# Kernel tuning notes

Hardware: AMD Instinct MI355X
Metric: run time of the kernel (lower is better)

The kernel has to match this reference:

```python
import jax, jax.numpy as jnp
import numpy as np

NC = 10          # num_clusters
D_MODEL = 512
H = 8
DK = 64          # d_model = H*DK
B = 8
L = 2048


def _mlp2(x, W1, b1, W2, b2):
    h = jax.nn.gelu(x @ W1 + b1, approximate=False)
    return h @ W2 + b2


def setup_inputs() -> dict:
    key = jax.random.key(0)
    ks = jax.random.split(key, 12)
    s_in = 1.0 / np.sqrt(D_MODEL)
    s_h = 1.0 / np.sqrt(4 * NC)
    s_nc = 1.0 / np.sqrt(NC)
    return {
        "Q": jax.random.normal(ks[0], (B, H, L, DK), jnp.float32),
        "K": jax.random.normal(ks[1], (B, H, L, DK), jnp.float32),
        "V": jax.random.normal(ks[2], (B, H, L, DK), jnp.float32),
        # cluster_k_proj: Linear(d_model,4*nc) GELU Linear(4*nc,nc); stored as [in,out]
        "Wk1": jax.random.normal(ks[3], (D_MODEL, 4 * NC), jnp.float32) * s_in,
        "bk1": jnp.zeros((4 * NC,), jnp.float32),
        "Wk2": jax.random.normal(ks[4], (4 * NC, NC), jnp.float32) * s_h,
        "bk2": jnp.zeros((NC,), jnp.float32),
        # cluster_q_proj
        "Wq1": jax.random.normal(ks[5], (D_MODEL, 4 * NC), jnp.float32) * s_in,
        "bq1": jnp.zeros((4 * NC,), jnp.float32),
        "Wq2": jax.random.normal(ks[6], (4 * NC, NC), jnp.float32) * s_h,
        "bq2": jnp.zeros((NC,), jnp.float32),
        # proj_back_to_cluster_k: Linear(nc, d_model) + GELU
        "Wp": jax.random.normal(ks[7], (NC, D_MODEL), jnp.float32) * s_nc,
        "bp": jnp.zeros((D_MODEL,), jnp.float32),
    }


def _forward(Q, K, V, Wk1, bk1, Wk2, bk2, Wq1, bq1, Wq2, bq2, Wp, bp):
    b, h, l, d_k = Q.shape
    nc = Wk2.shape[1]
    unfolding = 10 * nc

    def pool(x):
        # torch: MaxPool1d(kernel=9, stride=9(default), padding=4) on reshape(b, d_k*h, -1)
        x3 = x.reshape(b, d_k * h, -1)
        y = jax.lax.reduce_window(x3, -jnp.inf, jax.lax.max,
                                  (1, 1, 9), (1, 1, 9),
                                  ((0, 0), (0, 0), (4, 4)))
        return y.reshape(b, h, -1, d_k)

    Kp = pool(K)
    Vp = pool(V)
    l_k = Kp.shape[2]

    # pad along batch dim and take sliding windows of size `unfolding` (stride 1)
    pad = jnp.zeros((unfolding, h, l_k, d_k), Kp.dtype)
    K_padded = jnp.concatenate([pad, Kp[1:]], axis=0)      # [unfolding+b-1, h, l_k, d_k]
    idx = jnp.arange(b)[:, None] + jnp.arange(unfolding)[None, :]
    K_unf = K_padded[idx]                                  # [b, unfolding, h, l_k, d_k]
    K_unf = jnp.transpose(K_unf, (0, 2, 3, 4, 1))          # torch unfold puts window last
    K_unf = K_unf.reshape(b, l_k, unfolding, d_k * h)      # row-major reshape, as torch

    ck = jax.nn.softmax(_mlp2(K_unf, Wk1, bk1, Wk2, bk2), axis=-1)  # [b,l_k,u,nc]
    cq = jax.nn.softmax(_mlp2(K_unf, Wq1, bq1, Wq2, bq2), axis=-1)

    mu = jnp.mean(cq, axis=-1)                             # [b, l_k, unfolding]
    sigma = jax.nn.softplus(jnp.std(cq, axis=-1, ddof=1))  # torch std is unbiased
    x = jnp.mean(ck, axis=-1)
    log_prob = -0.5 * jnp.square((x - mu) / sigma) - jnp.log(sigma) - 0.5 * jnp.log(2.0 * jnp.pi)
    # torch CrossEntropyLoss(mu, mu): classes are dim 1 (l_k), soft prob targets
    logp = jax.nn.log_softmax(mu, axis=1)
    ce = jnp.mean(-jnp.sum(mu * logp, axis=1))
    loss = -jnp.mean(log_prob) + ce

    # fused scatter-style cluster centers: mean over window of cq with assigned cluster zeroed
    assign = jnp.argmax(cq, axis=-1)                       # [b, l_k, unfolding]
    onehot = jax.nn.one_hot(assign, nc, dtype=cq.dtype)    # [b, l_k, u, i] (constant wrt grad)
    total = jnp.sum(cq, axis=2)                            # [b, l_k, nc]
    S = jnp.einsum('blui,bluc->blic', onehot, cq)          # sum of cq at masked positions
    centers = (total[:, :, None, :] - S) / unfolding       # [b, l_k, nc_i, nc_c]
    centers = jnp.transpose(centers, (2, 0, 1, 3))         # [nc, b, l_k, nc]

    cc = jax.nn.gelu(centers @ Wp + bp, approximate=False) # [nc, b, l_k, d_model]
    cc = cc.reshape(b, h, nc, l_k, d_k)                    # faithful torch reshape

    scores = jnp.einsum('bhqd,bhckd->bhqk', Q, cc) / np.sqrt(d_k).astype(Q.dtype)
    attn = jax.nn.softmax(scores, axis=-1)
    context = jnp.einsum('bhqk,bhkd->bhqd', attn, Vp)
    return context, loss


def reference(Q, K, V, Wk1, bk1, Wk2, bk2, Wq1, bq1, Wq2, bq2, Wp, bp):
    return _forward(Q, K, V, Wk1, bk1, Wk2, bk2, Wq1, bq1, Wq2, bq2, Wp, bp)
```

## Files before the change

kernel.cpp:

```cpp
#include <hip/hip_runtime.h>
#include <math.h>

#define NCL 10
#define DM 512
#define NH 8
#define DK 64
#define NB 8
#define SL 2048
#define LK 228
#define UF 100
#define KP_PER_B (NH*LK*DK)
#define KP_TOT (NB*KP_PER_B)
#define NROWS (NB*LK*UF)
#define POOL2_BLOCKS 8192

typedef __bf16 bf16_t;
typedef __attribute__((ext_vector_type(2))) __bf16 bf16x2;
typedef __attribute__((ext_vector_type(8))) __bf16 bf16x8;
typedef __attribute__((ext_vector_type(4))) float f32x4;

__device__ __forceinline__ float gelu_f(float x) {
    return 0.5f * x * (1.f + erff(x * 0.70710678118654752f));
}

__global__ void k_pool(const float* __restrict__ K, const float* __restrict__ V,
                       float* __restrict__ Kp, float* __restrict__ Vp,
                       const float* __restrict__ Wq1, bf16_t* __restrict__ W1b,
                       float* __restrict__ acc) {
    int bid = blockIdx.x;
    int tid = threadIdx.x;
    if (bid >= POOL2_BLOCKS) {
        int i = (bid - POOL2_BLOCKS) * 256 + tid;
        if (i < 512 * 40) W1b[i] = (bf16_t)Wq1[i];
        if (bid == POOL2_BLOCKS && tid < 4) acc[tid] = 0.f;
        return;
    }
    int kv = bid >> 12;
    int e0 = bid & 4095;
    int b = e0 >> 9;
    int c = e0 & 511;
    const float* src = kv ? V : K;
    float* dst = kv ? Vp : Kp;
    __shared__ float buf[2048];
    const float* base = src + (size_t)e0 * 2048;
    #pragma unroll
    for (int i = 0; i < 2; ++i) {
        int i4 = (tid + i * 256) << 2;
        *(float4*)&buf[i4] = *(const float4*)&base[i4];
    }
    __syncthreads();
    if (tid < LK) {
        int p0 = tid * 9 - 4;
        float mx = -3.4e38f;
        #pragma unroll
        for (int j = 0; j < 9; ++j) {
            int p = p0 + j;
            if (p >= 0 && p < 2048) mx = fmaxf(mx, buf[p]);
        }
        dst[b * KP_PER_B + c * LK + tid] = mx;
    }
}

template<int B>
__device__ __forceinline__ void layer1(int tid, const bf16_t* __restrict__ W1b,
                                       const float* __restrict__ Sstf,
                                       float* __restrict__ hT) {
    #pragma unroll 1
    for (int k = 0; k < 2; ++k) {
        int vt = tid + (k << 8);
        if (vt < 500) {
            int m = vt / 5;
            int h8 = vt - m * 5;
            int bm = (12 * m) % 100;
            float h[8];
            #pragma unroll
            for (int i = 0; i < 8; ++i) h[i] = 0.f;
            #pragma unroll
            for (int s = 1; s <= B; ++s) {
                const int t = 99 - B + s;
                int d0 = t - bm; if (d0 < 0) d0 += 100;
                int r0 = ((m << 9) + d0 - t) / 100;
                const float* srow = &Sstf[(s - 1) << 9];
                #pragma unroll
                for (int j = 0; j < 6; ++j) {
                    int c = d0 + j * 100;
                    if (j < 5 || c < 512) {
                        float v = srow[r0 + j];
                        bf16x8 w = *(const bf16x8*)&W1b[c * 40 + h8 * 8];
                        #pragma unroll
                        for (int i = 0; i < 8; ++i)
                            h[i] = fmaf(v, (float)w[i], h[i]);
                    }
                }
            }
            #pragma unroll
            for (int i = 0; i < 8; ++i) hT[m * 44 + h8 * 8 + i] = h[i];
        }
    }
}

__global__ __launch_bounds__(256, 4) void k_mlp(
        const float* __restrict__ Kp, const bf16_t* __restrict__ W1b,
        const float* __restrict__ bq1,
        const float* __restrict__ Wq2, const float* __restrict__ bq2,
        float* __restrict__ mu_g, float* __restrict__ centers_g,
        float* __restrict__ acc_g) {
    __shared__ __align__(16) char smem[32384];
    float* Sstf  = (float*)smem;
    float* hT    = (float*)(smem + 14336);
    float* stats = (float*)(smem + 31936);

    int tid = threadIdx.x;
    int bid = blockIdx.x;
    int b = bid & 7;
    int l = bid >> 3;
    int bl = b * LK + l;

    for (int s4 = tid; s4 < 128 * b; s4 += 256) {
        int bk = (s4 >> 7) + 1;
        int r4 = (s4 & 127) << 2;
        *(float4*)&Sstf[((bk - 1) << 9) + r4] =
            *(const float4*)&Kp[bk * KP_PER_B + l * 512 + r4];
    }
    if (tid < 111) stats[tid] = 0.f;
    if (b == 0) {
        for (int i = tid; i < 4400; i += 256) hT[i] = 0.f;
    }
    __syncthreads();

    switch (b) {
        case 1: layer1<1>(tid, W1b, Sstf, hT); break;
        case 2: layer1<2>(tid, W1b, Sstf, hT); break;
        case 3: layer1<3>(tid, W1b, Sstf, hT); break;
        case 4: layer1<4>(tid, W1b, Sstf, hT); break;
        case 5: layer1<5>(tid, W1b, Sstf, hT); break;
        case 6: layer1<6>(tid, W1b, Sstf, hT); break;
        case 7: layer1<7>(tid, W1b, Sstf, hT); break;
        default: break;
    }
    __syncthreads();

    for (int i = tid; i < 4000; i += 256) {
        int row = i / 40;
        int j = i - row * 40;
        hT[row * 44 + j] = gelu_f(hT[row * 44 + j] + bq1[j]);
    }
    __syncthreads();

    float* total_l = stats;
    float* S_l = stats + 10;
    float* lp_acc = stats + 110;

    if (tid < 100) {
        int row = tid;
        float g[40];
        #pragma unroll
        for (int j4 = 0; j4 < 10; ++j4) {
            float4 gv = *(const float4*)&hT[row * 44 + j4 * 4];
            g[j4 * 4 + 0] = gv.x; g[j4 * 4 + 1] = gv.y;
            g[j4 * 4 + 2] = gv.z; g[j4 * 4 + 3] = gv.w;
        }
        float out[10];
        #pragma unroll
        for (int c = 0; c < 10; ++c) out[c] = bq2[c];
        #pragma unroll
        for (int j = 0; j < 40; ++j) {
            float gj = g[j];
            #pragma unroll
            for (int c = 0; c < 10; ++c)
                out[c] = fmaf(gj, Wq2[j * 10 + c], out[c]);
        }
        float m = out[0]; int am = 0;
        #pragma unroll
        for (int c = 1; c < 10; ++c)
            if (out[c] > m) { m = out[c]; am = c; }
        float e[10], s = 0.f;
        #pragma unroll
        for (int c = 0; c < 10; ++c) { e[c] = expf(out[c] - m); s += e[c]; }
        float inv = 1.f / s;
        float cq[10], s1 = 0.f;
        #pragma unroll
        for (int c = 0; c < 10; ++c) { cq[c] = e[c] * inv; s1 += cq[c]; }
        float mean = s1 * 0.1f;
        float var = 0.f;
        #pragma unroll
        for (int c = 0; c < 10; ++c) { float d = cq[c] - mean; var += d * d; }
        float sd = sqrtf(var / 9.f);
        float sp = log1pf(expf(sd));
        float lp = -logf(sp) - 0.91893853320467274f;
        mu_g[bl * 100 + row] = mean;
        atomicAdd(lp_acc, lp);
        #pragma unroll
        for (int c = 0; c < 10; ++c) {
            atomicAdd(&total_l[c], cq[c]);
            atomicAdd(&S_l[am * 10 + c], cq[c]);
        }
    }
    __syncthreads();
    if (tid == 0) atomicAdd(&acc_g[0], lp_acc[0]);
    if (tid < 100) {
        centers_g[bl * 100 + tid] = (total_l[tid % 10] - S_l[tid]) * 0.01f;
    }
}

__global__ void k_ce(const float* __restrict__ mu_g, float* __restrict__ acc_g,
                     float* __restrict__ outp) {
    int bid = blockIdx.x;
    int b = bid / 100;
    int u = bid % 100;
    int lane = threadIdx.x;
    float v[4];
    #pragma unroll
    for (int t = 0; t < 4; ++t) {
        int l = lane + t * 64;
        v[t] = (l < LK) ? mu_g[(b * LK + l) * 100 + u] : -3.4e38f;
    }
    float m = fmaxf(fmaxf(v[0], v[1]), fmaxf(v[2], v[3]));
    for (int o = 32; o > 0; o >>= 1) m = fmaxf(m, __shfl_xor(m, o, 64));
    float se = 0.f;
    #pragma unroll
    for (int t = 0; t < 4; ++t) {
        int l = lane + t * 64;
        if (l < LK) se += expf(v[t] - m);
    }
    for (int o = 32; o > 0; o >>= 1) se += __shfl_xor(se, o, 64);
    float lse = m + logf(se);
    float dot = 0.f;
    #pragma unroll
    for (int t = 0; t < 4; ++t) {
        int l = lane + t * 64;
        if (l < LK) dot += v[t] * (v[t] - lse);
    }
    for (int o = 32; o > 0; o >>= 1) dot += __shfl_xor(dot, o, 64);
    if (lane == 0) {
        atomicAdd(&acc_g[1], -dot * (1.f / 800.f));
        __threadfence();
        unsigned int old = atomicAdd((unsigned int*)&acc_g[2], 1u);
        if (old == 799u) {
            __threadfence();
            outp[8388608] = -(acc_g[0] * (1.f / (float)NROWS)) + acc_g[1];
        }
    }
}

__global__ void k_ccs(const float* __restrict__ centers_g,
                      const float* __restrict__ Wp, const float* __restrict__ bp,
                      float* __restrict__ ccs) {
    int tid = blockIdx.x * 256 + threadIdx.x;
    if (tid >= KP_TOT) return;
    int k2d2 = tid % (LK * DK);
    int bh = tid / (LK * DK);
    float s = 0.f;
    #pragma unroll
    for (int i2 = 0; i2 < 10; ++i2) {
        int t2 = bh * 145920 + i2 * 14592 + k2d2;
        int i = t2 / 933888;
        int r1 = t2 % 933888;
        int bs = r1 / 116736;
        int r2 = r1 % 116736;
        int ls = r2 / 512;
        int mm = r2 % 512;
        const float* cen = centers_g + (bs * LK + ls) * 100 + i * 10;
        float val = bp[mm];
        #pragma unroll
        for (int c = 0; c < 10; ++c)
            val = fmaf(cen[c], Wp[c * 512 + mm], val);
        s += gelu_f(val);
    }
    ccs[tid] = s;
}

#define QT 128
__global__ __launch_bounds__(256, 3) void k_attn(
        const float* __restrict__ Q, const float* __restrict__ ccs,
        const float* __restrict__ Vp, float* __restrict__ outp) {
    __shared__ __align__(16) char smem[36864];
    bf16_t* Kl = (bf16_t*)(smem);
    bf16_t* Vt = (bf16_t*)(smem + 9216);
    bf16_t* Pl = (bf16_t*)(smem + 18432);

    int tid = threadIdx.x;
    int wid = tid >> 6;
    int lane = tid & 63;
    int ln = lane & 15;
    int qd = lane >> 4;
    int bid = blockIdx.x;
    int bh = bid >> 4;
    int qt = bid & 15;
    int qbase = qt * QT;

    const float* Qbh = Q + (size_t)bh * SL * DK;
    const float* Kbh = ccs + (size_t)bh * LK * DK;
    const float* Vbh = Vp + (size_t)bh * LK * DK;

    for (int s = tid; s < QT * 32; s += 256) {
        int r = s >> 5;
        int c2 = s & 31;
        float2 v = *(const float2*)&Qbh[(size_t)(qbase + r) * DK + c2 * 2];
        *(bf16x2*)&Pl[r * 72 + c2 * 2] = (bf16x2){(bf16_t)v.x, (bf16_t)v.y};
    }
    __syncthreads();
    bf16x8 qf[2][2];
    #pragma unroll
    for (int mt = 0; mt < 2; ++mt)
        #pragma unroll
        for (int ks = 0; ks < 2; ++ks)
            qf[mt][ks] = *(const bf16x8*)&Pl[(wid * 32 + mt * 16 + ln) * 72 + ks * 32 + qd * 8];

    f32x4 acc_o[2][4];
    float mrow[2][4], lrow[2][4];
    #pragma unroll
    for (int mt = 0; mt < 2; ++mt)
        #pragma unroll
        for (int t = 0; t < 4; ++t) {
            acc_o[mt][t] = (f32x4)(0.f);
            mrow[mt][t] = -3.0e38f;
            lrow[mt][t] = 0.f;
        }

    for (int ch = 0; ch < 4; ++ch) {
        int k0 = ch * 64;
        __syncthreads();
        for (int s = tid; s < 64 * 32; s += 256) {
            int kk = s >> 5;
            int c2 = s & 31;
            int key = k0 + kk;
            float2 v = (key < LK) ? *(const float2*)&Kbh[(size_t)key * DK + c2 * 2]
                                  : make_float2(0.f, 0.f);
            *(bf16x2*)&Kl[kk * 72 + c2 * 2] = (bf16x2){(bf16_t)v.x, (bf16_t)v.y};
        }
        for (int s = tid; s < 64 * 16; s += 256) {
            int kk = s >> 4;
            int c4 = s & 15;
            int key = k0 + kk;
            float4 v = (key < LK) ? *(const float4*)&Vbh[(size_t)key * DK + c4 * 4]
                                  : make_float4(0.f, 0.f, 0.f, 0.f);
            Vt[(c4 * 4 + 0) * 72 + kk] = (bf16_t)v.x;
            Vt[(c4 * 4 + 1) * 72 + kk] = (bf16_t)v.y;
            Vt[(c4 * 4 + 2) * 72 + kk] = (bf16_t)v.z;
            Vt[(c4 * 4 + 3) * 72 + kk] = (bf16_t)v.w;
        }
        __syncthreads();

        f32x4 accs[2][4];
        #pragma unroll
        for (int mt = 0; mt < 2; ++mt)
            #pragma unroll
            for (int nt = 0; nt < 4; ++nt) accs[mt][nt] = (f32x4)(0.f);
        #pragma unroll
        for (int ks = 0; ks < 2; ++ks) {
            #pragma unroll
            for (int nt = 0; nt < 4; ++nt) {
                bf16x8 bf = *(const bf16x8*)&Kl[(nt * 16 + ln) * 72 + ks * 32 + qd * 8];
                #pragma unroll
                for (int mt = 0; mt < 2; ++mt)
                    accs[mt][nt] = __builtin_amdgcn_mfma_f32_16x16x32_bf16(qf[mt][ks], bf, accs[mt][nt], 0, 0, 0);
            }
        }

        #pragma unroll
        for (int mt = 0; mt < 2; ++mt) {
            #pragma unroll
            for (int r = 0; r < 4; ++r) {
                float sv[4];
                #pragma unroll
                for (int nt = 0; nt < 4; ++nt) {
                    float s = accs[mt][nt][r] * 0.125f;
                    int key = k0 + nt * 16 + ln;
                    sv[nt] = (key < LK) ? s : -3.0e38f;
                }
                float rmax = fmaxf(fmaxf(sv[0], sv[1]), fmaxf(sv[2], sv[3]));
                #pragma unroll
                for (int o = 1; o < 16; o <<= 1)
                    rmax = fmaxf(rmax, __shfl_xor(rmax, o, 64));
                float mold = mrow[mt][r];
                float mnew = fmaxf(mold, rmax);
                float alpha = __expf(mold - mnew);
                float p[4], psum = 0.f;
                #pragma unroll
                for (int nt = 0; nt < 4; ++nt) {
                    p[nt] = __expf(sv[nt] - mnew);
                    psum += p[nt];
                }
                #pragma unroll
                for (int o = 1; o < 16; o <<= 1)
                    psum += __shfl_xor(psum, o, 64);
                lrow[mt][r] = lrow[mt][r] * alpha + psum;
                mrow[mt][r] = mnew;
                #pragma unroll
                for (int ntv = 0; ntv < 4; ++ntv)
                    acc_o[mt][ntv][r] *= alpha;
                int prow = (wid * 32 + mt * 16 + qd * 4 + r) * 72;
                #pragma unroll
                for (int nt = 0; nt < 4; ++nt)
                    Pl[prow + nt * 16 + ln] = (bf16_t)p[nt];
            }
        }

        #pragma unroll
        for (int ks = 0; ks < 2; ++ks) {
            bf16x8 pa[2];
            #pragma unroll
            for (int mt = 0; mt < 2; ++mt)
                pa[mt] = *(const bf16x8*)&Pl[(wid * 32 + mt * 16 + ln) * 72 + ks * 32 + qd * 8];
            #pragma unroll
            for (int ntv = 0; ntv < 4; ++ntv) {
                bf16x8 vb = *(const bf16x8*)&Vt[(ntv * 16 + ln) * 72 + ks * 32 + qd * 8];
                #pragma unroll
                for (int mt = 0; mt < 2; ++mt)
                    acc_o[mt][ntv] = __builtin_amdgcn_mfma_f32_16x16x32_bf16(pa[mt], vb, acc_o[mt][ntv], 0, 0, 0);
            }
        }
    }

    #pragma unroll
    for (int mt = 0; mt < 2; ++mt) {
        #pragma unroll
        for (int r = 0; r < 4; ++r) {
            float inv = 1.f / lrow[mt][r];
            int q_idx = qbase + wid * 32 + mt * 16 + qd * 4 + r;
            float* orow = outp + ((size_t)bh * SL + q_idx) * DK;
            #pragma unroll
            for (int ntv = 0; ntv < 4; ++ntv)
                orow[ntv * 16 + ln] = acc_o[mt][ntv][r] * inv;
        }
    }
}

extern "C" void kernel_launch(void* const* d_in, const int* in_sizes, int n_in,
                              void* d_out, int out_size, void* d_ws, size_t ws_size,
                              hipStream_t stream) {
    const float* Q   = (const float*)d_in[0];
    const float* K   = (const float*)d_in[1];
    const float* V   = (const float*)d_in[2];
    const float* Wq1 = (const float*)d_in[7];
    const float* bq1 = (const float*)d_in[8];
    const float* Wq2 = (const float*)d_in[9];
    const float* bq2 = (const float*)d_in[10];
    const float* Wp  = (const float*)d_in[11];
    const float* bp  = (const float*)d_in[12];
    float* out = (float*)d_out;

    float* ws      = (float*)d_ws;
    float* Kp      = ws;
    float* Vp      = ws + 933888;
    float* mu      = ws + 1867776;
    float* centers = ws + 2050176;
    float* ccs     = ws + 2232576;
    float* acc     = ws + 3166464;
    bf16_t* W1b    = (bf16_t*)(ws + 3166468);

    k_pool<<<POOL2_BLOCKS + 80, 256, 0, stream>>>(K, V, Kp, Vp, Wq1, W1b, acc);
    k_mlp<<<NB * LK, 256, 0, stream>>>(Kp, W1b, bq1, Wq2, bq2, mu, centers, acc);
    k_ccs<<<(KP_TOT + 255) / 256, 256, 0, stream>>>(centers, Wp, bp, ccs);
    k_ce<<<NB * 100, 64, 0, stream>>>(mu, acc, out);
    k_attn<<<NB * NH * (SL / QT), 256, 0, stream>>>(Q, ccs, Vp, out);
}
```

Before: 331.3 us.

## Fuse ccs and CE kernels, transpose mu layout, prescale Q, raise attn occupancy

Merges the ccs projection kernel and the cross-entropy kernel into one launch, with block ranges dispatching to each part. This removes one launch and lets the two independent pieces of work overlap. The mu buffer is stored transposed so the CE reduction reads it contiguously instead of with a stride of 100. The ccs index math now uses shifts and masks instead of divisions, and the 1/sqrt(dk) scale moves into the Q load so it leaves the inner loop. The attention kernel's launch bounds go from 3 to 4 blocks per SM, which may force register spills.

Measured after the change: 324.7 us. -2.0%, faster.

```diff
diff --git a/kernel.cpp b/kernel.cpp
--- a/kernel.cpp
+++ b/kernel.cpp
@@ -13,6 +13,8 @@
 #define KP_TOT (NB*KP_PER_B)
 #define NROWS (NB*LK*UF)
 #define POOL2_BLOCKS 8192
+#define KCCS_BLOCKS 3648
+#define KCE_BLOCKS 200
 
 typedef __bf16 bf16_t;
 typedef __attribute__((ext_vector_type(2))) __bf16 bf16x2;
@@ -188,7 +190,7 @@
         float sd = sqrtf(var / 9.f);
         float sp = log1pf(expf(sd));
         float lp = -logf(sp) - 0.91893853320467274f;
-        mu_g[bl * 100 + row] = mean;
+        mu_g[(b * 100 + row) * LK + l] = mean;
         atomicAdd(lp_acc, lp);
         #pragma unroll
         for (int c = 0; c < 10; ++c) {
@@ -203,17 +205,46 @@
     }
 }
 
-__global__ void k_ce(const float* __restrict__ mu_g, float* __restrict__ acc_g,
-                     float* __restrict__ outp) {
+__global__ void k_ccs_ce(const float* __restrict__ centers_g,
+                         const float* __restrict__ Wp, const float* __restrict__ bp,
+                         float* __restrict__ ccs,
+                         const float* __restrict__ mu_g, float* __restrict__ acc_g,
+                         float* __restrict__ outp) {
     int bid = blockIdx.x;
-    int b = bid / 100;
-    int u = bid % 100;
-    int lane = threadIdx.x;
+    if (bid < KCCS_BLOCKS) {
+        int tid = bid * 256 + threadIdx.x;
+        int k2d2 = tid % (LK * DK);
+        int bh = tid / (LK * DK);
+        float s = 0.f;
+        #pragma unroll
+        for (int i2 = 0; i2 < 10; ++i2) {
+            int J  = bh * 10 + i2;
+            int i  = J >> 6;
+            int Jm = J & 63;
+            int bs = Jm >> 3;
+            int r2 = (Jm & 7) * 14592 + k2d2;
+            int ls = r2 >> 9;
+            int mm = r2 & 511;
+            const float* cen = centers_g + (bs * LK + ls) * 100 + i * 10;
+            float val = bp[mm];
+            #pragma unroll
+            for (int c = 0; c < 10; ++c)
+                val = fmaf(cen[c], Wp[c * 512 + mm], val);
+            s += gelu_f(val);
+        }
+        ccs[tid] = s;
+        return;
+    }
+    int unit = (bid - KCCS_BLOCKS) * 4 + (threadIdx.x >> 6);
+    int b = unit / 100;
+    int u = unit % 100;
+    int lane = threadIdx.x & 63;
+    const float* murow = mu_g + (b * 100 + u) * LK;
     float v[4];
     #pragma unroll
     for (int t = 0; t < 4; ++t) {
         int l = lane + t * 64;
-        v[t] = (l < LK) ? mu_g[(b * LK + l) * 100 + u] : -3.4e38f;
+        v[t] = (l < LK) ? murow[l] : -3.4e38f;
     }
     float m = fmaxf(fmaxf(v[0], v[1]), fmaxf(v[2], v[3]));
     for (int o = 32; o > 0; o >>= 1) m = fmaxf(m, __shfl_xor(m, o, 64));
@@ -243,35 +274,8 @@
     }
 }
 
-__global__ void k_ccs(const float* __restrict__ centers_g,
-                      const float* __restrict__ Wp, const float* __restrict__ bp,
-                      float* __restrict__ ccs) {
-    int tid = blockIdx.x * 256 + threadIdx.x;
-    if (tid >= KP_TOT) return;
-    int k2d2 = tid % (LK * DK);
-    int bh = tid / (LK * DK);
-    float s = 0.f;
-    #pragma unroll
-    for (int i2 = 0; i2 < 10; ++i2) {
-        int t2 = bh * 145920 + i2 * 14592 + k2d2;
-        int i = t2 / 933888;
-        int r1 = t2 % 933888;
-        int bs = r1 / 116736;
-        int r2 = r1 % 116736;
-        int ls = r2 / 512;
-        int mm = r2 % 512;
-        const float* cen = centers_g + (bs * LK + ls) * 100 + i * 10;
-        float val = bp[mm];
-        #pragma unroll
-        for (int c = 0; c < 10; ++c)
-            val = fmaf(cen[c], Wp[c * 512 + mm], val);
-        s += gelu_f(val);
-    }
-    ccs[tid] = s;
-}
-
 #define QT 128
-__global__ __launch_bounds__(256, 3) void k_attn(
+__global__ __launch_bounds__(256, 4) void k_attn(
         const float* __restrict__ Q, const float* __restrict__ ccs,
         const float* __restrict__ Vp, float* __restrict__ outp) {
     __shared__ __align__(16) char smem[36864];
@@ -297,7 +301,8 @@
         int r = s >> 5;
         int c2 = s & 31;
         float2 v = *(const float2*)&Qbh[(size_t)(qbase + r) * DK + c2 * 2];
-        *(bf16x2*)&Pl[r * 72 + c2 * 2] = (bf16x2){(bf16_t)v.x, (bf16_t)v.y};
+        *(bf16x2*)&Pl[r * 72 + c2 * 2] =
+            (bf16x2){(bf16_t)(v.x * 0.125f), (bf16_t)(v.y * 0.125f)};
     }
     __syncthreads();
     bf16x8 qf[2][2];
@@ -365,7 +370,7 @@
                 float sv[4];
                 #pragma unroll
                 for (int nt = 0; nt < 4; ++nt) {
-                    float s = accs[mt][nt][r] * 0.125f;
+                    float s = accs[mt][nt][r];
                     int key = k0 + nt * 16 + ln;
                     sv[nt] = (key < LK) ? s : -3.0e38f;
                 }
@@ -452,7 +457,7 @@
 
     k_pool<<<POOL2_BLOCKS + 80, 256, 0, stream>>>(K, V, Kp, Vp, Wq1, W1b, acc);
     k_mlp<<<NB * LK, 256, 0, stream>>>(Kp, W1b, bq1, Wq2, bq2, mu, centers, acc);
-    k_ccs<<<(KP_TOT + 255) / 256, 256, 0, stream>>>(centers, Wp, bp, ccs);
-    k_ce<<<NB * 100, 64, 0, stream>>>(mu, acc, out);
+    k_ccs_ce<<<KCCS_BLOCKS + KCE_BLOCKS, 256, 0, stream>>>(centers, Wp, bp, ccs,
+                                                           mu, acc, out);
     k_attn<<<NB * NH * (SL / QT), 256, 0, stream>>>(Q, ccs, Vp, out);
 }
```
